# Kernel tuning notes

Measured on AMD Instinct MI355X. Metric: run time of the kernel, lower is better.

Reference implementation:

```python
import itertools
import jax, jax.numpy as jnp
import numpy as np


def setup_inputs() -> dict:
    key = jax.random.key(0)
    k1, k2 = jax.random.split(key)
    B = 4
    F = (128, 128, 128)  # fixed image grid
    M = (128, 128, 128)  # moving image dims
    ddf = jax.random.normal(k1, (B, *F, 3), dtype=jnp.float32)
    image = jax.random.normal(k2, (B, *M), dtype=jnp.float32)
    return {"ddf": ddf, "image": image}


def _warp(image, ddf):
    # image: (B, m1, m2, m3); ddf: (B, f1, f2, f3, 3)
    B = image.shape[0]
    m_dims = image.shape[1:4]
    f_dims = ddf.shape[1:4]
    # reference grid in voxel coordinates of the fixed image
    grid = jnp.stack(
        jnp.meshgrid(*(jnp.arange(s, dtype=ddf.dtype) for s in f_dims), indexing="ij"),
        axis=-1,
    )  # (f1, f2, f3, 3)
    loc = grid[None] + ddf  # sample locations in moving-image voxel coords
    max_f = jnp.asarray([d - 1 for d in m_dims], dtype=ddf.dtype)
    loc = jnp.clip(loc, 0.0, max_f)  # boundary clamp (as in neurite resample)
    loc0 = jnp.floor(loc)
    w1 = loc - loc0  # trilinear weights toward the upper corner
    i0 = loc0.astype(jnp.int32)
    i1 = jnp.minimum(i0 + 1, jnp.asarray([d - 1 for d in m_dims], dtype=jnp.int32))
    bidx = jnp.arange(B)[:, None, None, None]
    out = jnp.zeros((B,) + f_dims, dtype=image.dtype)
    # 8-corner gather + weighted sum
    for corner in itertools.product((0, 1), repeat=3):
        idx = [(i1 if corner[a] else i0)[..., a] for a in range(3)]
        w = jnp.ones((), dtype=image.dtype)
        for a in range(3):
            w = w * (w1[..., a] if corner[a] else (1.0 - w1[..., a]))
        out = out + w * image[bidx, idx[0], idx[1], idx[2]]
    return out


def reference(ddf, image):
    return _warp(image, ddf)
```

## Files before the change

### kernel.cpp

```cpp
#include <hip/hip_runtime.h>


#define DIM 128
#define HALO 4
#define RX 17
#define RY 17
#define ZP 28
#define PLANE (RY * ZP)
#define RSZ 8192

typedef float vfloat4 __attribute__((ext_vector_type(4)));

__global__ __launch_bounds__(256) void warp_kernel(
    const float* __restrict__ ddf,
    const float* __restrict__ image,
    float* __restrict__ out)
{
    __shared__ float tile[RSZ];

    int bid = blockIdx.x;
    int zb = bid & 7;
    int yb = (bid >> 3) & 15;
    int xb = (bid >> 7) & 15;
    int b  = bid >> 11;

    int x0 = xb << 3, y0 = yb << 3, z0 = zb << 4;

    int rx0 = min(max(x0 - HALO, 0), DIM - RX);
    int ry0 = min(max(y0 - HALO, 0), DIM - RY);
    int rz0 = min(max(z0 - HALO, 0), DIM - ZP);

    int tid = threadIdx.x;

    int txy = tid >> 2;
    int x = x0 + (txy >> 3);
    int y = y0 + (txy & 7);
    int zbase = z0 + ((tid & 3) << 2);
    int v0 = (b << 21) + (x << 14) + (y << 7) + zbase;

    const vfloat4* dv = (const vfloat4*)(ddf + (size_t)v0 * 3);
    vfloat4 p0 = __builtin_nontemporal_load(dv + 0);
    vfloat4 p1 = __builtin_nontemporal_load(dv + 1);
    vfloat4 p2 = __builtin_nontemporal_load(dv + 2);

    const float* img = image + ((size_t)b << 21);

    {
        int base0 = (rx0 << 14) + (ry0 << 7) + rz0;
        int t4 = tid << 2;
#pragma unroll
        for (int k = 0; k < 8; ++k) {
            int i = (k << 10) + t4;
            int rx  = i / PLANE;
            int rem = i - rx * PLANE;
            int ry  = rem / ZP;
            int rz  = rem - ry * ZP;
            int goff = base0 + (rx << 14) + (ry << 7) + rz;
            goff = min(goff, (1 << 21) - 4);
            __builtin_amdgcn_global_load_lds(
                (const __attribute__((address_space(1))) void*)(img + goff),
                (__attribute__((address_space(3))) void*)(tile + i),
                16, 0, 0);
        }
    }
    __syncthreads();

    float dxl[4] = {p0.x, p0.w, p1.z, p2.y};
    float dyl[4] = {p0.y, p1.x, p1.w, p2.z};
    float dzl[4] = {p0.z, p1.y, p2.x, p2.w};

    const float maxf = (float)(DIM - 1);
    vfloat4 r;

#pragma unroll
    for (int j = 0; j < 4; ++j) {
        float lx = (float)x + dxl[j];
        float ly = (float)y + dyl[j];
        float lz = (float)(zbase + j) + dzl[j];
        lx = fminf(fmaxf(lx, 0.0f), maxf);
        ly = fminf(fmaxf(ly, 0.0f), maxf);
        lz = fminf(fmaxf(lz, 0.0f), maxf);
        float fx = floorf(lx), fy = floorf(ly), fz = floorf(lz);
        int ix0 = (int)fx, iy0 = (int)fy, iz0 = (int)fz;
        int ix1 = min(ix0 + 1, DIM - 1);
        int iy1 = min(iy0 + 1, DIM - 1);
        int iz1 = min(iz0 + 1, DIM - 1);
        float wx1 = lx - fx, wy1 = ly - fy, wz1 = lz - fz;

        bool inReg = (ix0 >= rx0) & (ix1 <= rx0 + RX - 1)
                   & (iy0 >= ry0) & (iy1 <= ry0 + RY - 1)
                   & (iz0 >= rz0) & (iz1 <= rz0 + ZP - 1);

        float c000, c001, c010, c011, c100, c101, c110, c111;
        if (inReg) {
            int la  = (ix0 - rx0) * PLANE + (iy0 - ry0) * ZP + (iz0 - rz0);
            int ddx = (ix1 - ix0) * PLANE;
            int ddy = (iy1 - iy0) * ZP;
            int ddz = (iz1 - iz0);
            c000 = tile[la];             c001 = tile[la + ddz];
            c010 = tile[la + ddy];       c011 = tile[la + ddy + ddz];
            c100 = tile[la + ddx];       c101 = tile[la + ddx + ddz];
            c110 = tile[la + ddx + ddy]; c111 = tile[la + ddx + ddy + ddz];
        } else {
            int bx0 = ix0 << 14, bx1 = ix1 << 14;
            int by0 = iy0 << 7,  by1 = iy1 << 7;
            c000 = img[bx0 + by0 + iz0]; c001 = img[bx0 + by0 + iz1];
            c010 = img[bx0 + by1 + iz0]; c011 = img[bx0 + by1 + iz1];
            c100 = img[bx1 + by0 + iz0]; c101 = img[bx1 + by0 + iz1];
            c110 = img[bx1 + by1 + iz0]; c111 = img[bx1 + by1 + iz1];
        }

        float c00 = __builtin_fmaf(wz1, c001 - c000, c000);
        float c01 = __builtin_fmaf(wz1, c011 - c010, c010);
        float c10 = __builtin_fmaf(wz1, c101 - c100, c100);
        float c11 = __builtin_fmaf(wz1, c111 - c110, c110);
        float c0  = __builtin_fmaf(wy1, c01 - c00, c00);
        float c1  = __builtin_fmaf(wy1, c11 - c10, c10);
        r[j]      = __builtin_fmaf(wx1, c1 - c0, c0);
    }

    __builtin_nontemporal_store(r, (vfloat4*)(out + v0));
}

extern "C" void kernel_launch(void* const* d_in, const int* in_sizes, int n_in,
                              void* d_out, int out_size, void* d_ws, size_t ws_size,
                              hipStream_t stream) {
    const float* ddf   = (const float*)d_in[0];
    const float* image = (const float*)d_in[1];
    float* out = (float*)d_out;

    int grid = 4 * 16 * 16 * 8;
    warp_kernel<<<grid, 256, 0, stream>>>(ddf, image, out);
}
```

Baseline: 206.7 us.

## Enlarge tiles to 16x8x16 with 512 threads and remap thread-to-voxel layout

```diff
diff --git a/kernel.cpp b/kernel.cpp
--- a/kernel.cpp
+++ b/kernel.cpp
@@ -3,15 +3,16 @@
 
 #define DIM 128
 #define HALO 4
-#define RX 17
-#define RY 17
-#define ZP 28
-#define PLANE (RY * ZP)
-#define RSZ 8192
+#define RXT 25
+#define RYT 17
+#define ZP  28
+#define PLANE (RYT * ZP)
+#define REAL  (RXT * PLANE)
+#define RSZ  12288
 
 typedef float vfloat4 __attribute__((ext_vector_type(4)));
 
-__global__ __launch_bounds__(256) void warp_kernel(
+__global__ __launch_bounds__(512, 6) void warp_kernel(
     const float* __restrict__ ddf,
     const float* __restrict__ image,
     float* __restrict__ out)
@@ -19,29 +20,36 @@
     __shared__ float tile[RSZ];
 
     int bid = blockIdx.x;
-    int zb = bid & 7;
-    int yb = (bid >> 3) & 15;
-    int xb = (bid >> 7) & 15;
-    int b  = bid >> 11;
+    int zt = bid & 7;
+    int yt = (bid >> 3) & 15;
+    int xt = (bid >> 7) & 7;
+    int b  = bid >> 10;
 
-    int x0 = xb << 3, y0 = yb << 3, z0 = zb << 4;
+    int x0 = xt << 4, y0 = yt << 3, z0 = zt << 4;
 
-    int rx0 = min(max(x0 - HALO, 0), DIM - RX);
-    int ry0 = min(max(y0 - HALO, 0), DIM - RY);
+    int rx0 = min(max(x0 - HALO, 0), DIM - RXT);
+    int ry0 = min(max(y0 - HALO, 0), DIM - RYT);
     int rz0 = min(max(z0 - HALO, 0), DIM - ZP);
 
     int tid = threadIdx.x;
 
-    int txy = tid >> 2;
-    int x = x0 + (txy >> 3);
-    int y = y0 + (txy & 7);
-    int zbase = z0 + ((tid & 3) << 2);
-    int v0 = (b << 21) + (x << 14) + (y << 7) + zbase;
+    int zs = tid & 15;
+    int yy = (tid >> 4) & 7;
+    int xp = tid >> 7;
 
-    const vfloat4* dv = (const vfloat4*)(ddf + (size_t)v0 * 3);
-    vfloat4 p0 = __builtin_nontemporal_load(dv + 0);
-    vfloat4 p1 = __builtin_nontemporal_load(dv + 1);
-    vfloat4 p2 = __builtin_nontemporal_load(dv + 2);
+    int x = x0 + xp;
+    int y = y0 + yy;
+    int z = z0 + zs;
+    int vbase = (b << 21) + (x << 14) + (y << 7) + z;
+
+    float d0[4], d1[4], d2[4];
+#pragma unroll
+    for (int j = 0; j < 4; ++j) {
+        const float* dp = ddf + (size_t)3 * (unsigned)(vbase + ((j << 2) << 14));
+        d0[j] = __builtin_nontemporal_load(dp);
+        d1[j] = __builtin_nontemporal_load(dp + 1);
+        d2[j] = __builtin_nontemporal_load(dp + 2);
+    }
 
     const float* img = image + ((size_t)b << 21);
 
@@ -49,8 +57,8 @@
         int base0 = (rx0 << 14) + (ry0 << 7) + rz0;
         int t4 = tid << 2;
 #pragma unroll
-        for (int k = 0; k < 8; ++k) {
-            int i = (k << 10) + t4;
+        for (int k = 0; k < 6; ++k) {
+            int i = (k << 11) + t4;
             int rx  = i / PLANE;
             int rem = i - rx * PLANE;
             int ry  = rem / ZP;
@@ -65,18 +73,14 @@
     }
     __syncthreads();
 
-    float dxl[4] = {p0.x, p0.w, p1.z, p2.y};
-    float dyl[4] = {p0.y, p1.x, p1.w, p2.z};
-    float dzl[4] = {p0.z, p1.y, p2.x, p2.w};
-
     const float maxf = (float)(DIM - 1);
-    vfloat4 r;
 
 #pragma unroll
     for (int j = 0; j < 4; ++j) {
-        float lx = (float)x + dxl[j];
-        float ly = (float)y + dyl[j];
-        float lz = (float)(zbase + j) + dzl[j];
+        int xj = x + (j << 2);
+        float lx = (float)xj + d0[j];
+        float ly = (float)y  + d1[j];
+        float lz = (float)z  + d2[j];
         lx = fminf(fmaxf(lx, 0.0f), maxf);
         ly = fminf(fmaxf(ly, 0.0f), maxf);
         lz = fminf(fmaxf(lz, 0.0f), maxf);
@@ -87,8 +91,8 @@
         int iz1 = min(iz0 + 1, DIM - 1);
         float wx1 = lx - fx, wy1 = ly - fy, wz1 = lz - fz;
 
-        bool inReg = (ix0 >= rx0) & (ix1 <= rx0 + RX - 1)
-                   & (iy0 >= ry0) & (iy1 <= ry0 + RY - 1)
+        bool inReg = (ix0 >= rx0) & (ix1 <= rx0 + RXT - 1)
+                   & (iy0 >= ry0) & (iy1 <= ry0 + RYT - 1)
                    & (iz0 >= rz0) & (iz1 <= rz0 + ZP - 1);
 
         float c000, c001, c010, c011, c100, c101, c110, c111;
@@ -116,10 +120,10 @@
         float c11 = __builtin_fmaf(wz1, c111 - c110, c110);
         float c0  = __builtin_fmaf(wy1, c01 - c00, c00);
         float c1  = __builtin_fmaf(wy1, c11 - c10, c10);
-        r[j]      = __builtin_fmaf(wx1, c1 - c0, c0);
+        float r   = __builtin_fmaf(wx1, c1 - c0, c0);
+
+        __builtin_nontemporal_store(r, out + vbase + ((j << 2) << 14));
     }
-
-    __builtin_nontemporal_store(r, (vfloat4*)(out + v0));
 }
 
 extern "C" void kernel_launch(void* const* d_in, const int* in_sizes, int n_in,
@@ -129,6 +133,6 @@
     const float* image = (const float*)d_in[1];
     float* out = (float*)d_out;
 
-    int grid = 4 * 16 * 16 * 8;
-    warp_kernel<<<grid, 256, 0, stream>>>(ddf, image, out);
+    int grid = 4 * 8 * 16 * 8;
+    warp_kernel<<<grid, 512, 0, stream>>>(ddf, image, out);
 }
```

After: 192.8 us. 6.7% less time.
